# Kernel optimization log

Hardware: AMD Instinct MI355X
Metric: run time of the kernel (lower is better)

The kernel has to match this reference:

```python
import jax, jax.numpy as jnp
import numpy as np

NUM_HOPS = 2
GAMMA = 0.8


def setup_inputs() -> dict:
    key = jax.random.key(0)
    ks = jax.random.split(key, 17)
    B, L, V, E, M, Mt, R = 8, 128, 50257, 768, 400, 800, 40
    W = 0.02  # init scale for learned params
    return {
        'hidden_states': jax.random.normal(ks[0], (B, L, E), jnp.float32),
        'wte': jax.random.normal(ks[1], (V, E), jnp.float32) * W,
        'rel_emb': jax.random.normal(ks[2], (R, E), jnp.float32) * W,
        'W_s': jax.random.normal(ks[3], (NUM_HOPS, E, E), jnp.float32) * W,
        'W_n': jax.random.normal(ks[4], (NUM_HOPS, E, E), jnp.float32) * W,
        'W_r': jax.random.normal(ks[5], (NUM_HOPS, E, E), jnp.float32) * W,
        'W_triple': jax.random.normal(ks[6], (E, 3 * E), jnp.float32) * W,
        'gate_w': jax.random.normal(ks[7], (E,), jnp.float32) * W,
        'gate_b': jnp.zeros((), jnp.float32),
        'concept_ids': jax.random.randint(ks[8], (B, M), 0, V),
        'relation_ids': jax.random.randint(ks[9], (B, Mt), 0, R),
        'head_idx': jax.random.randint(ks[10], (B, Mt), 0, M),
        'tail_idx': jax.random.randint(ks[11], (B, Mt), 0, M),
        'triple_labels': jax.random.randint(ks[12], (B, Mt), 0, 2),
        'distances': jax.random.randint(ks[13], (B, M), 0, 3),
        'vocab_map': jax.random.randint(ks[14], (V,), 0, M),
        'map_mask': jax.random.randint(ks[15], (V,), 0, 2),
    }


def _triple_encoder(wte, rel_emb, W_s, W_n, W_r, concept_ids, relation_ids, head_idx, tail_idx):
    concept_repr = wte[concept_ids]      # B,M,E
    rel_repr = rel_emb[relation_ids]     # B,Mt,E

    def gcn(cr, rr, h, t):               # per-batch CompGCN, faithful to torch loop
        M = cr.shape[0]
        ch, rh = cr, rr
        for l in range(NUM_HOPS):
            upd = jnp.zeros_like(cr)
            upd = upd.at[t].add(cr[h] - rr)   # scatter_add(o) + scatter_add(-rel)
            upd = upd.at[h].add(cr[t] - rr)
            cnt = jnp.zeros((M,), cr.dtype).at[t].add(1.0).at[h].add(1.0)
            upd = cr @ W_s[l].T + (upd @ W_n[l].T) / jnp.clip(cnt, 1.0, None)[:, None]
            ch = jax.nn.relu(upd)
            rh = rr @ W_r[l].T
        return ch, rh

    node, relh = jax.vmap(gcn)(concept_repr, rel_repr, head_idx, tail_idx)
    E = node.shape[-1]
    hi = jnp.broadcast_to(head_idx[:, :, None], head_idx.shape + (E,))
    ti = jnp.broadcast_to(tail_idx[:, :, None], tail_idx.shape + (E,))
    hrep = jnp.take_along_axis(node, hi, axis=1)
    trep = jnp.take_along_axis(node, ti, axis=1)
    return jnp.concatenate([hrep, relh, trep], axis=-1)  # B,Mt,3E


def _multi_hop(triple_prob, distances, head, tail):
    B, L, Mt = triple_prob.shape
    M = distances.shape[1]
    dt = triple_prob.dtype
    init_mask = jnp.broadcast_to((distances == 0).astype(dt)[:, None, :], (B, L, M))
    decay = (0.8 ** distances.astype(dt))[:, None, :]
    head_b = jnp.broadcast_to(head[:, None, :], (B, L, Mt))

    def scatter_mean(vals, t):  # vals: L,Mt  t: Mt -> L,M
        s = jnp.zeros((L, M), vals.dtype).at[:, t].add(vals)
        c = jnp.zeros((M,), vals.dtype).at[t].add(1.0)
        return s / jnp.clip(c, 1.0, None)

    node_score = init_mask
    total = init_mask * (-100000.0)
    for _ in range(NUM_HOPS):
        ths = jnp.take_along_axis(node_score, head_b, axis=2)  # B,L,Mt
        upd = ths * GAMMA + triple_prob
        node_score = jax.vmap(scatter_mean)(upd, tail)          # B,L,M
        total = total + node_score * decay
    return total


def reference(hidden_states, wte, rel_emb, W_s, W_n, W_r, W_triple, gate_w, gate_b,
              concept_ids, relation_ids, head_idx, tail_idx, triple_labels,
              distances, vocab_map, map_mask):
    triple_repr = _triple_encoder(wte, rel_emb, W_s, W_n, W_r,
                                  concept_ids, relation_ids, head_idx, tail_idx)
    lm_probs = jax.nn.softmax(hidden_states @ wte.T, axis=-1)            # B,L,V
    tl = triple_repr @ W_triple.T                                        # B,Mt,E
    triple_prob = jax.nn.sigmoid(jnp.einsum('ble,bme->blm', hidden_states, tl))
    triple_prob = triple_prob * (triple_labels != -1)[:, None, :].astype(triple_prob.dtype)
    scores = _multi_hop(triple_prob, distances, head_idx, tail_idx)      # B,L,M
    concept_probs = jax.nn.softmax(scores, axis=-1)
    cpv = concept_probs[:, :, vocab_map]                                 # gather into vocab: B,L,V
    cpv = cpv * (map_mask != 0)[None, None, :].astype(cpv.dtype)
    gate = jax.nn.sigmoid(hidden_states @ gate_w + gate_b)[..., None]    # B,L,1
    probs = gate * cpv + (1.0 - gate) * lm_probs
    return probs
```

## Files before the change

kernel.cpp:

```cpp
#include <hip/hip_runtime.h>
#include <stdint.h>

#define HB 8
#define HL 128
#define HV 50257
#define HE 768
#define HM 400
#define HMT 800
#define HBL (HB*HL)
#define NTILES 393
#define ELD 50272
#define WTE_F4 ((long)HV*HE/4)

typedef __attribute__((ext_vector_type(4))) float f32x4;
typedef __attribute__((ext_vector_type(8))) short bf16x8;
typedef unsigned short u16;

struct u16x4 { u16 x, y, z, w; };

__device__ __forceinline__ u16 f2bf(float x){
  union { float f; uint32_t u; } v; v.f = x;
  uint32_t r = v.u + 0x7fffu + ((v.u >> 16) & 1u);
  return (u16)(r >> 16);
}
__device__ __forceinline__ float bf2f(u16 b){
  union { uint32_t u; float f; } v; v.u = ((uint32_t)b) << 16;
  return v.f;
}
__device__ __forceinline__ void glds(const u16* g, const u16* l){
  __builtin_amdgcn_global_load_lds(
      (const __attribute__((address_space(1))) void*)g,
      (__attribute__((address_space(3))) void*)l, 16, 0, 0);
}
__device__ __forceinline__ void cvt_slice(const float* __restrict__ src,
    u16* __restrict__ dst, long lo4, long n4, int relb, int nb){
  long i = lo4 + (long)relb*256 + threadIdx.x;
  const long end = lo4 + n4;
  const long stride = (long)nb*256;
  for (; i < end; i += stride) {
    float4 x = ((const float4*)src)[i];
    u16x4 y; y.x=f2bf(x.x); y.y=f2bf(x.y); y.z=f2bf(x.z); y.w=f2bf(x.w);
    ((u16x4*)dst)[i] = y;
  }
}

__global__ __launch_bounds__(256) void prep_k(const float* __restrict__ hs,
    const float* __restrict__ rel, const float* __restrict__ Wr1src,
    const float* __restrict__ Wt, const float* __restrict__ Ws1,
    const float* __restrict__ Wn1, const int* __restrict__ vmap,
    const int* __restrict__ mmask,
    u16* __restrict__ hid_b, u16* __restrict__ rel_b,
    u16* __restrict__ wr1, u16* __restrict__ wtT, u16* __restrict__ wcat,
    int* __restrict__ vmm){
  const int b = blockIdx.x, t = threadIdx.x;
  if (b < 768) {
    int i = b*256 + t;
    float4 x = ((const float4*)hs)[i];
    u16x4 y; y.x=f2bf(x.x); y.y=f2bf(x.y); y.z=f2bf(x.z); y.w=f2bf(x.w);
    ((u16x4*)hid_b)[i] = y;
  } else if (b < 798) {
    int i = (b-768)*256 + t;
    float4 x = ((const float4*)rel)[i];
    u16x4 y; y.x=f2bf(x.x); y.y=f2bf(x.y); y.z=f2bf(x.z); y.w=f2bf(x.w);
    ((u16x4*)rel_b)[i] = y;
  } else if (b < 1374) {
    int i = (b-798)*256 + t;
    float4 x = ((const float4*)Wr1src)[i];
    u16x4 y; y.x=f2bf(x.x); y.y=f2bf(x.y); y.z=f2bf(x.z); y.w=f2bf(x.w);
    ((u16x4*)wr1)[i] = y;
  } else if (b < 3102) {
    int g = (b-1374)*256 + t;
    int f = g / 192, r = g - f*192, e0 = r*4;
    u16x4 y;
    y.x = f2bf(Wt[(long)(e0+0)*2304 + f]);
    y.y = f2bf(Wt[(long)(e0+1)*2304 + f]);
    y.z = f2bf(Wt[(long)(e0+2)*2304 + f]);
    y.w = f2bf(Wt[(long)(e0+3)*2304 + f]);
    *(u16x4*)&wtT[(long)f*HE + e0] = y;
  } else if (b < 5406) {
    int i = (b-3102)*256 + t;
    int e = i / HE, k = i - e*HE;
    wcat[(long)e*(2*HE) + k]      = f2bf(Ws1[i]);
    wcat[(long)e*(2*HE) + HE + k] = f2bf(Wn1[i]);
  } else {
    int base = (b-5406)*1024 + t*4;
    #pragma unroll
    for (int i = 0; i < 4; ++i) {
      int c = base + i;
      if (c < HV) vmm[c] = mmask[c] ? vmap[c] : -1;
    }
  }
}

__global__ __launch_bounds__(256) void gcn_scatter_k(const float* __restrict__ wte,
    const float* __restrict__ rel, const int* __restrict__ cids,
    const int* __restrict__ rids, const int* __restrict__ head,
    const int* __restrict__ tail, u16* __restrict__ An,
    u16* __restrict__ wte_b){
  if (blockIdx.x >= 384) {
    cvt_slice(wte, wte_b, 0, 3145728L, blockIdx.x - 384, 3072);
    return;
  }
  const int ch = blockIdx.x % 48;
  const int b  = blockIdx.x / 48;
  const int e0 = ch * 16;
  __shared__ float cw[HM][17];
  __shared__ float upd[HM][17];
  __shared__ float relc[40][17];
  __shared__ float cnt[HM];
  const int tid = threadIdx.x;

  for (int idx = tid; idx < HM*16; idx += 256) {
    int m = idx >> 4, e = idx & 15;
    cw[m][e] = wte[(long)cids[b*HM+m]*HE + e0 + e];
    upd[m][e] = 0.f;
  }
  for (int idx = tid; idx < 40*16; idx += 256) {
    int r = idx >> 4, e = idx & 15;
    relc[r][e] = rel[r*HE + e0 + e];
  }
  for (int m = tid; m < HM; m += 256) cnt[m] = 0.f;
  __syncthreads();

  for (int j = tid; j < HMT; j += 256) {
    int h = head[b*HMT+j], t = tail[b*HMT+j], r = rids[b*HMT+j];
    atomicAdd(&cnt[t], 1.f);
    atomicAdd(&cnt[h], 1.f);
    #pragma unroll
    for (int e = 0; e < 16; ++e) {
      float rv = relc[r][e];
      atomicAdd(&upd[t][e], cw[h][e] - rv);
      atomicAdd(&upd[h][e], cw[t][e] - rv);
    }
  }
  __syncthreads();

  for (int idx = tid; idx < HM*16; idx += 256) {
    int m = idx >> 4, e = idx & 15;
    float ic = 1.f / fmaxf(cnt[m], 1.f);
    u16* dst = An + ((long)b*HM + m) * (2*HE);
    dst[e0 + e]      = f2bf(cw[m][e]);
    dst[HE + e0 + e] = f2bf(upd[m][e] * ic);
  }
}

template<int ACT, int OUTBF16, int BIG, int DBUF>
__device__ __forceinline__ void gemm_core(
    const u16* __restrict__ Ab, const u16* __restrict__ Bb,
    void* __restrict__ Cout, float* __restrict__ rowpart,
    int Mdim, int Ndim, int Kdim, int lda, int ldb, int ldc,
    int mtile, int ntile, u16* AsmB, u16* BsmB)
{
  const int m0 = mtile * 128;
  const int n0 = ntile * 128;
  const int tid = threadIdx.x;
  const int lane = tid & 63;
  const int wid = tid >> 6;
  const int wr = wid >> 1, wc = wid & 1;
  const int srw = lane >> 3;
  const int sl  = lane & 7;

  f32x4 acc[4][4] = {};

  auto stage = [&](int buf, int k0) {
    u16* As = AsmB + buf*8192;
    u16* Bs = BsmB + buf*8192;
    #pragma unroll
    for (int i = 0; i < 4; ++i) {
      const int c = i*4 + wid;
      const int row = c*8 + srw;
      const int koff = k0 + ((sl ^ srw) * 8);
      int ra = m0 + row; if (ra > Mdim-1) ra = Mdim-1;
      glds(Ab + (long)ra * lda + koff, &As[c*512]);
      int rn = n0 + row; if (rn > Ndim-1) rn = Ndim-1;
      glds(Bb + (long)rn * ldb + koff, &Bs[c*512]);
    }
  };
  auto compute = [&](int buf) {
    const u16* As = AsmB + buf*8192;
    const u16* Bs = BsmB + buf*8192;
    #pragma unroll
    for (int kk = 0; kk < 2; ++kk) {
      bf16x8 af[4], bfr[4];
      #pragma unroll
      for (int mi = 0; mi < 4; ++mi) {
        const int R = wr*64 + mi*16 + (lane & 15);
        af[mi] = *(const bf16x8*)&As[R*64 + (((kk*4 + (lane>>4)) ^ (R & 7)) * 8)];
      }
      #pragma unroll
      for (int ni = 0; ni < 4; ++ni) {
        const int R = wc*64 + ni*16 + (lane & 15);
        bfr[ni] = *(const bf16x8*)&Bs[R*64 + (((kk*4 + (lane>>4)) ^ (R & 7)) * 8)];
      }
      #pragma unroll
      for (int mi = 0; mi < 4; ++mi)
        #pragma unroll
        for (int ni = 0; ni < 4; ++ni)
          acc[mi][ni] = __builtin_amdgcn_mfma_f32_16x16x32_bf16(af[mi], bfr[ni], acc[mi][ni], 0, 0, 0);
    }
  };

  const int NT = Kdim >> 6;
  if (DBUF) {
    stage(0, 0);
    __syncthreads();
    int cur = 0;
    for (int t = 0; t < NT; ++t) {
      if (t + 1 < NT) stage(cur ^ 1, (t + 1) << 6);
      compute(cur);
      __syncthreads();
      cur ^= 1;
    }
  } else {
    for (int t = 0; t < NT; ++t) {
      stage(0, t << 6);
      __syncthreads();
      compute(0);
      __syncthreads();
    }
  }

  const int cr0 = m0 + wr*64 + ((lane >> 4) * 4);
  const int cc0 = n0 + wc*64 + (lane & 15);

  if (BIG) {
    float* rs = (float*)AsmB;
    #pragma unroll
    for (int mi = 0; mi < 4; ++mi) {
      #pragma unroll
      for (int r = 0; r < 4; ++r) {
        const int rowi = cr0 + mi*16 + r;
        float s = 0.f;
        #pragma unroll
        for (int ni = 0; ni < 4; ++ni) {
          const int col = cc0 + ni*16;
          if (col < Ndim) {
            float e = __expf(acc[mi][ni][r]);
            if (OUTBF16) ((u16*)Cout)[(long)rowi*ELD + col] = f2bf(e);
            else        ((float*)Cout)[(long)rowi*HV + col] = e;
            s += e;
          }
        }
        s += __shfl_xor(s, 8); s += __shfl_xor(s, 4);
        s += __shfl_xor(s, 2); s += __shfl_xor(s, 1);
        if ((lane & 15) == 0)
          rs[wc*128 + wr*64 + mi*16 + ((lane >> 4) << 2) + r] = s;
      }
    }
    __syncthreads();
    if (tid < 128)
      rowpart[(long)(m0 + tid) * NTILES + ntile] = rs[tid] + rs[128 + tid];
    return;
  }

  #pragma unroll
  for (int mi = 0; mi < 4; ++mi) {
    #pragma unroll
    for (int ni = 0; ni < 4; ++ni) {
      const int col = cc0 + ni*16;
      if (col < Ndim) {
        #pragma unroll
        for (int r = 0; r < 4; ++r) {
          const int rowi = cr0 + mi*16 + r;
          if (rowi < Mdim) {
            float v = acc[mi][ni][r];
            if (ACT == 1) v = fmaxf(v, 0.f);
            if (OUTBF16) ((u16*)Cout)[(long)rowi*ldc + col] = f2bf(v);
            else        ((float*)Cout)[(long)rowi*ldc + col] = v;
          }
        }
      }
    }
  }
}

template<int EXPBF>
__global__ __launch_bounds__(256) void gemm_big(
    const u16* __restrict__ hid_b, const u16* __restrict__ wte_b,
    void* __restrict__ expl, float* __restrict__ rowpart,
    int Mdim, int Ndim, int Kdim, int lda, int ldb, int ldc)
{
  __shared__ alignas(16) u16 Asm[8192];
  __shared__ alignas(16) u16 Bsm[8192];
  const int wg = (blockIdx.x & 7) * NTILES + (blockIdx.x >> 3);
  gemm_core<0,EXPBF,1,0>(hid_b, wte_b, expl, rowpart,
      Mdim, Ndim, Kdim, lda, ldb, ldc, wg & 7, wg >> 3, Asm, Bsm);
}

__global__ __launch_bounds__(256) void gemm_multi0(
    const u16* __restrict__ anode, const u16* __restrict__ wcat,
    u16* __restrict__ nodeb, const u16* __restrict__ rel_b,
    const u16* __restrict__ wr1, u16* __restrict__ relWr,
    const u16* __restrict__ hid_b, const u16* __restrict__ wtT,
    u16* __restrict__ hw, const float* __restrict__ wte,
    u16* __restrict__ wte_b)
{
  if (blockIdx.x >= 342) {
    cvt_slice(wte, wte_b, 3145728L, 4194304L, blockIdx.x - 342, 4096);
    return;
  }
  __shared__ alignas(16) u16 Asm[2*8192];
  __shared__ alignas(16) u16 Bsm[2*8192];
  const int q = blockIdx.x;
  if (q < 192) {
    const int z = q / 24, r = q - z*24;
    gemm_core<1,1,0,1>(anode + (long)z*HM*2*HE, wcat, nodeb + (long)z*HM*HE,
        nullptr, HM, HE, 2*HE, 2*HE, 2*HE, HE, r & 3, r >> 2, Asm, Bsm);
  } else if (q < 198) {
    gemm_core<0,1,0,1>(rel_b, wr1, relWr, nullptr,
        40, HE, HE, HE, HE, HE, 0, q - 192, Asm, Bsm);
  } else {
    const int u = q - 198;
    gemm_core<0,1,0,1>(hid_b, wtT, hw, nullptr,
        HBL, 3*HE, HE, HE, HE, 3*HE, u & 7, u >> 3, Asm, Bsm);
  }
}

__global__ __launch_bounds__(256) void gemm_multi1(
    const u16* __restrict__ hw, const u16* __restrict__ nodeb,
    const u16* __restrict__ relWr, float* __restrict__ scores,
    const float* __restrict__ wte, u16* __restrict__ wte_b)
{
  if (blockIdx.x >= 72) {
    cvt_slice(wte, wte_b, 7340032L, 1048576L, blockIdx.x - 72, 1024);
    return;
  }
  __shared__ alignas(16) u16 Asm[2*8192];
  __shared__ alignas(16) u16 Bsm[2*8192];
  const int q = blockIdx.x;
  if (q < 32) {
    const int z = q >> 2;
    gemm_core<0,0,0,1>(hw + (long)z*HL*(3*HE), nodeb + (long)z*HM*HE,
        scores + (long)z*HL*840, nullptr,
        HL, HM, HE, 3*HE, HE, 840, 0, q & 3, Asm, Bsm);
  } else if (q < 64) {
    const int z = (q - 32) >> 2;
    gemm_core<0,0,0,1>(hw + (long)z*HL*(3*HE) + 2*HE, nodeb + (long)z*HM*HE,
        scores + (long)z*HL*840 + HM, nullptr,
        HL, HM, HE, 3*HE, HE, 840, 0, (q - 32) & 3, Asm, Bsm);
  } else {
    gemm_core<0,0,0,1>(hw + HE, relWr, scores + 2*HM, nullptr,
        HBL, 40, HE, 3*HE, HE, 840, q - 64, 0, Asm, Bsm);
  }
}

__global__ __launch_bounds__(256) void multihop_k(const float* __restrict__ scores,
    const float* __restrict__ hs, const float* __restrict__ gw,
    const float* __restrict__ gb,
    const int* __restrict__ head, const int* __restrict__ tail,
    const int* __restrict__ rids, const int* __restrict__ labels,
    const int* __restrict__ dist, float* __restrict__ gatev,
    float* __restrict__ cprob, const float* __restrict__ wte,
    u16* __restrict__ wte_b){
  if (blockIdx.x >= HBL) {
    cvt_slice(wte, wte_b, 8388608L, WTE_F4 - 8388608L, blockIdx.x - HBL, 1280);
    return;
  }
  const int bl = blockIdx.x;
  const int b = bl >> 7;
  const int tid = threadIdx.x;
  const int lane = tid & 63, wid = tid >> 6;
  __shared__ float srow[840];
  __shared__ float tp[HMT];
  __shared__ float ns[HM], sacc[HM], tot[HM], invc[HM], dec[HM];
  __shared__ float red[16];
  __shared__ float gred[4];
  const int* hb = head + b*HMT;
  const int* tb = tail + b*HMT;
  const int* rb = rids + b*HMT;
  const int* lb = labels + b*HMT;
  const float* sr = scores + (long)bl * 840;

  float gs = 0.f;
  for (int e = tid; e < HE; e += 256) gs += hs[(long)bl*HE + e] * gw[e];
  for (int o = 32; o; o >>= 1) gs += __shfl_down(gs, o);
  if (lane == 0) gred[wid] = gs;

  for (int i = tid; i < 840; i += 256) srow[i] = sr[i];
  for (int m = tid; m < HM; m += 256) {
    int d = dist[b*HM + m];
    float im = (d == 0) ? 1.f : 0.f;
    ns[m] = im; tot[m] = im * -100000.f;
    dec[m] = (d == 0) ? 1.f : ((d == 1) ? 0.8f : 0.64f);
    sacc[m] = 0.f; invc[m] = 0.f;
  }
  __syncthreads();
  if (tid == 0)
    gatev[bl] = 1.f / (1.f + __expf(-(gred[0]+gred[1]+gred[2]+gred[3] + gb[0])));
  for (int j = tid; j < HMT; j += 256) {
    atomicAdd(&invc[tb[j]], 1.f);
    float x = srow[hb[j]] + srow[HM + tb[j]] + srow[2*HM + rb[j]];
    tp[j] = (lb[j] == -1) ? 0.f : 1.f / (1.f + __expf(-x));
  }
  __syncthreads();
  for (int m = tid; m < HM; m += 256) invc[m] = 1.f / fmaxf(invc[m], 1.f);
  __syncthreads();

  for (int hop = 0; hop < 2; ++hop) {
    for (int j = tid; j < HMT; j += 256) {
      float u = ns[hb[j]] * 0.8f + tp[j];
      atomicAdd(&sacc[tb[j]], u);
    }
    __syncthreads();
    for (int m = tid; m < HM; m += 256) {
      float v = sacc[m] * invc[m];
      ns[m] = v; tot[m] += v * dec[m]; sacc[m] = 0.f;
    }
    __syncthreads();
  }

  float lmx = -3.4e38f;
  for (int m = tid; m < HM; m += 256) lmx = fmaxf(lmx, tot[m]);
  for (int o = 32; o; o >>= 1) lmx = fmaxf(lmx, __shfl_down(lmx, o));
  if (lane == 0) red[wid] = lmx;
  __syncthreads();
  float gmx = fmaxf(fmaxf(red[0], red[1]), fmaxf(red[2], red[3]));
  float ls = 0.f;
  for (int m = tid; m < HM; m += 256) ls += __expf(tot[m] - gmx);
  for (int o = 32; o; o >>= 1) ls += __shfl_down(ls, o);
  if (lane == 0) red[8 + wid] = ls;
  __syncthreads();
  float inv = 1.f / (red[8] + red[9] + red[10] + red[11]);
  float* outrow = cprob + (long)bl * HM;
  for (int m = tid; m < HM; m += 256) outrow[m] = __expf(tot[m] - gmx) * inv;
}

template<int EXPBF>
__global__ __launch_bounds__(256) void finalize_k(const void* __restrict__ expl,
    const float* __restrict__ rowpart, const float* __restrict__ gatev,
    const float* __restrict__ cprob, const int* __restrict__ vmm,
    float* __restrict__ out){
  const int r = blockIdx.x / 13;
  const int ch = blockIdx.x - r*13;
  const int tid = threadIdx.x;
  __shared__ float red[4];
  __shared__ float cpl[HM];
  float s = 0.f;
  for (int t = tid; t < NTILES; t += 256) s += rowpart[r*NTILES + t];
  for (int o = 32; o; o >>= 1) s += __shfl_down(s, o);
  if ((tid & 63) == 0) red[tid >> 6] = s;
  const float g = gatev[r];
  for (int m = tid; m < HM; m += 256) cpl[m] = g * cprob[r*HM + m];
  __syncthreads();
  const float scale = (1.f - g) / (red[0] + red[1] + red[2] + red[3]);
  const u16* erb = (const u16*)expl + (long)r * ELD;
  const float* erf = (const float*)expl + (long)r * HV;
  float* orow = out + (long)r * HV;
  #pragma unroll
  for (int it = 0; it < 2; ++it) {
    const int c = ch*4096 + it*2048 + tid*8;
    if (c + 8 <= HV) {
      float e[8];
      if (EXPBF) {
        bf16x8 v = *(const bf16x8*)&erb[c];
        #pragma unroll
        for (int i = 0; i < 8; ++i) e[i] = bf2f((u16)v[i]);
      } else {
        float4 a = *(const float4*)&erf[c];
        float4 b2 = *(const float4*)&erf[c+4];
        e[0]=a.x; e[1]=a.y; e[2]=a.z; e[3]=a.w;
        e[4]=b2.x; e[5]=b2.y; e[6]=b2.z; e[7]=b2.w;
      }
      int4 v0 = *(const int4*)&vmm[c];
      int4 v1 = *(const int4*)&vmm[c+4];
      const int ix[8] = {v0.x, v0.y, v0.z, v0.w, v1.x, v1.y, v1.z, v1.w};
      float o8[8];
      #pragma unroll
      for (int i = 0; i < 8; ++i)
        o8[i] = (ix[i] >= 0 ? cpl[ix[i]] : 0.f) + scale * e[i];
      *(float4*)&orow[c]   = make_float4(o8[0], o8[1], o8[2], o8[3]);
      *(float4*)&orow[c+4] = make_float4(o8[4], o8[5], o8[6], o8[7]);
    } else if (c < HV) {
      for (int i = 0; i < 8 && c + i < HV; ++i) {
        float e = EXPBF ? bf2f(((const u16*)expl)[(long)r*ELD + c + i]) : erf[c+i];
        int ix = vmm[c+i];
        orow[c+i] = (ix >= 0 ? cpl[ix] : 0.f) + scale * e;
      }
    }
  }
}

extern "C" void kernel_launch(void* const* d_in, const int* in_sizes, int n_in,
                              void* d_out, int out_size, void* d_ws, size_t ws_size,
                              hipStream_t stream)
{
  const float* hs   = (const float*)d_in[0];
  const float* wte  = (const float*)d_in[1];
  const float* rel  = (const float*)d_in[2];
  const float* Ws   = (const float*)d_in[3];
  const float* Wn   = (const float*)d_in[4];
  const float* Wr   = (const float*)d_in[5];
  const float* Wt   = (const float*)d_in[6];
  const float* gw   = (const float*)d_in[7];
  const float* gb   = (const float*)d_in[8];
  const int* cids   = (const int*)d_in[9];
  const int* rids   = (const int*)d_in[10];
  const int* head   = (const int*)d_in[11];
  const int* tail   = (const int*)d_in[12];
  const int* labels = (const int*)d_in[13];
  const int* dist   = (const int*)d_in[14];
  const int* vmap   = (const int*)d_in[15];
  const int* mmask  = (const int*)d_in[16];
  float* out = (float*)d_out;

  char* ws = (char*)d_ws;
  size_t o = 0;
  auto alloc = [&](size_t bytes) -> char* {
    char* p = ws + o; o = (o + bytes + 255) & ~(size_t)255; return p;
  };
  u16* wte_b     = (u16*)alloc((size_t)HV*HE*2);
  u16* hid_b     = (u16*)alloc((size_t)HBL*HE*2);
  float* cprob   = (float*)alloc((size_t)HBL*HM*4);
  float* rowpart = (float*)alloc((size_t)HBL*NTILES*4);
  float* gatev   = (float*)alloc(HBL*4);
  int* vmm       = (int*)alloc((size_t)HV*4);
  float* scores  = (float*)alloc((size_t)HBL*840*4);

  const bool bigws = ws_size >= (size_t)196*1024*1024;
  u16* expl = (u16*)(ws + o);
  u16* wcat  = (u16*)alloc((size_t)HE*2*HE*2);
  u16* wr1   = (u16*)alloc((size_t)HE*HE*2);
  u16* wtT   = (u16*)alloc((size_t)3*HE*HE*2);
  u16* rel_b = (u16*)alloc((size_t)40*HE*2);
  u16* anode = (u16*)alloc((size_t)HB*HM*2*HE*2);
  u16* nodeb = (u16*)alloc((size_t)HB*HM*HE*2);
  u16* relWr = (u16*)alloc((size_t)40*HE*2);
  u16* hw    = (u16*)alloc((size_t)HBL*3*HE*2);
  (void)in_sizes; (void)n_in; (void)out_size;

  prep_k<<<5456, 256, 0, stream>>>(hs, rel, Wr + (size_t)HE*HE, Wt,
      Ws + (size_t)HE*HE, Wn + (size_t)HE*HE, vmap, mmask,
      hid_b, rel_b, wr1, wtT, wcat, vmm);

  gcn_scatter_k<<<384 + 3072, 256, 0, stream>>>(wte, rel, cids, rids, head,
      tail, anode, wte_b);

  gemm_multi0<<<342 + 4096, 256, 0, stream>>>(anode, wcat, nodeb, rel_b, wr1,
      relWr, hid_b, wtT, hw, wte, wte_b);
  gemm_multi1<<<72 + 1024, 256, 0, stream>>>(hw, nodeb, relWr, scores,
      wte, wte_b);

  multihop_k<<<HBL + 1280, 256, 0, stream>>>(scores, hs, gw, gb, head, tail,
      rids, labels, dist, gatev, cprob, wte, wte_b);

  if (bigws) {
    gemm_big<1><<<3144, 256, 0, stream>>>(hid_b, wte_b, expl, rowpart,
        HBL, HV, HE, HE, HE, ELD);
    finalize_k<1><<<HBL*13, 256, 0, stream>>>(expl, rowpart, gatev, cprob,
        vmm, out);
  } else {
    gemm_big<0><<<3144, 256, 0, stream>>>(hid_b, wte_b, out, rowpart,
        HBL, HV, HE, HE, HE, HV);
    finalize_k<0><<<HBL*13, 256, 0, stream>>>(out, rowpart, gatev, cprob,
        vmm, out);
  }
}
```

Measured before the change: 398.1 us.

## Specialize big vocab GEMM with K=32 double-buffered tiles, merge prep and scatter kernels

The large logits GEMM gets its own kernel. It uses double-buffered K=32 stages through direct global-to-LDS loads and swaps the MFMA operands so each lane holds four consecutive columns, which allows vectorized 4-wide exp stores and a cheaper row-sum reduction. The prep kernel and the GCN scatter kernel are merged into a single launch to cut one kernel boundary. The wte conversion slices are rebalanced across the preceding launches. The changes trade LDS footprint and sync frequency (more K iterations) for overlap and wider stores.

```diff
diff --git a/kernel.cpp b/kernel.cpp
--- a/kernel.cpp
+++ b/kernel.cpp
@@ -44,61 +44,61 @@
   }
 }
 
-__global__ __launch_bounds__(256) void prep_k(const float* __restrict__ hs,
-    const float* __restrict__ rel, const float* __restrict__ Wr1src,
+__global__ __launch_bounds__(256) void gcn_prep_k(const float* __restrict__ wte,
+    const float* __restrict__ rel, const int* __restrict__ cids,
+    const int* __restrict__ rids, const int* __restrict__ head,
+    const int* __restrict__ tail, u16* __restrict__ An,
+    const float* __restrict__ hs, const float* __restrict__ Wr1src,
     const float* __restrict__ Wt, const float* __restrict__ Ws1,
     const float* __restrict__ Wn1, const int* __restrict__ vmap,
     const int* __restrict__ mmask,
     u16* __restrict__ hid_b, u16* __restrict__ rel_b,
     u16* __restrict__ wr1, u16* __restrict__ wtT, u16* __restrict__ wcat,
-    int* __restrict__ vmm){
-  const int b = blockIdx.x, t = threadIdx.x;
-  if (b < 768) {
-    int i = b*256 + t;
-    float4 x = ((const float4*)hs)[i];
-    u16x4 y; y.x=f2bf(x.x); y.y=f2bf(x.y); y.z=f2bf(x.z); y.w=f2bf(x.w);
-    ((u16x4*)hid_b)[i] = y;
-  } else if (b < 798) {
-    int i = (b-768)*256 + t;
-    float4 x = ((const float4*)rel)[i];
-    u16x4 y; y.x=f2bf(x.x); y.y=f2bf(x.y); y.z=f2bf(x.z); y.w=f2bf(x.w);
-    ((u16x4*)rel_b)[i] = y;
-  } else if (b < 1374) {
-    int i = (b-798)*256 + t;
-    float4 x = ((const float4*)Wr1src)[i];
-    u16x4 y; y.x=f2bf(x.x); y.y=f2bf(x.y); y.z=f2bf(x.z); y.w=f2bf(x.w);
-    ((u16x4*)wr1)[i] = y;
-  } else if (b < 3102) {
-    int g = (b-1374)*256 + t;
-    int f = g / 192, r = g - f*192, e0 = r*4;
-    u16x4 y;
-    y.x = f2bf(Wt[(long)(e0+0)*2304 + f]);
-    y.y = f2bf(Wt[(long)(e0+1)*2304 + f]);
-    y.z = f2bf(Wt[(long)(e0+2)*2304 + f]);
-    y.w = f2bf(Wt[(long)(e0+3)*2304 + f]);
-    *(u16x4*)&wtT[(long)f*HE + e0] = y;
-  } else if (b < 5406) {
-    int i = (b-3102)*256 + t;
-    int e = i / HE, k = i - e*HE;
-    wcat[(long)e*(2*HE) + k]      = f2bf(Ws1[i]);
-    wcat[(long)e*(2*HE) + HE + k] = f2bf(Wn1[i]);
-  } else {
-    int base = (b-5406)*1024 + t*4;
-    #pragma unroll
-    for (int i = 0; i < 4; ++i) {
-      int c = base + i;
-      if (c < HV) vmm[c] = mmask[c] ? vmap[c] : -1;
-    }
-  }
-}
-
-__global__ __launch_bounds__(256) void gcn_scatter_k(const float* __restrict__ wte,
-    const float* __restrict__ rel, const int* __restrict__ cids,
-    const int* __restrict__ rids, const int* __restrict__ head,
-    const int* __restrict__ tail, u16* __restrict__ An,
-    u16* __restrict__ wte_b){
+    int* __restrict__ vmm, u16* __restrict__ wte_b){
+  const int t = threadIdx.x;
+  if (blockIdx.x >= 5840) {
+    cvt_slice(wte, wte_b, 0, 2621440L, blockIdx.x - 5840, 2048);
+    return;
+  }
   if (blockIdx.x >= 384) {
-    cvt_slice(wte, wte_b, 0, 3145728L, blockIdx.x - 384, 3072);
+    const int b = blockIdx.x - 384;
+    if (b < 768) {
+      int i = b*256 + t;
+      float4 x = ((const float4*)hs)[i];
+      u16x4 y; y.x=f2bf(x.x); y.y=f2bf(x.y); y.z=f2bf(x.z); y.w=f2bf(x.w);
+      ((u16x4*)hid_b)[i] = y;
+    } else if (b < 798) {
+      int i = (b-768)*256 + t;
+      float4 x = ((const float4*)rel)[i];
+      u16x4 y; y.x=f2bf(x.x); y.y=f2bf(x.y); y.z=f2bf(x.z); y.w=f2bf(x.w);
+      ((u16x4*)rel_b)[i] = y;
+    } else if (b < 1374) {
+      int i = (b-798)*256 + t;
+      float4 x = ((const float4*)Wr1src)[i];
+      u16x4 y; y.x=f2bf(x.x); y.y=f2bf(x.y); y.z=f2bf(x.z); y.w=f2bf(x.w);
+      ((u16x4*)wr1)[i] = y;
+    } else if (b < 3102) {
+      int g = (b-1374)*256 + t;
+      int f = g / 192, r = g - f*192, e0 = r*4;
+      u16x4 y;
+      y.x = f2bf(Wt[(long)(e0+0)*2304 + f]);
+      y.y = f2bf(Wt[(long)(e0+1)*2304 + f]);
+      y.z = f2bf(Wt[(long)(e0+2)*2304 + f]);
+      y.w = f2bf(Wt[(long)(e0+3)*2304 + f]);
+      *(u16x4*)&wtT[(long)f*HE + e0] = y;
+    } else if (b < 5406) {
+      int i = (b-3102)*256 + t;
+      int e = i / HE, k = i - e*HE;
+      wcat[(long)e*(2*HE) + k]      = f2bf(Ws1[i]);
+      wcat[(long)e*(2*HE) + HE + k] = f2bf(Wn1[i]);
+    } else {
+      int base = (b-5406)*1024 + t*4;
+      #pragma unroll
+      for (int i = 0; i < 4; ++i) {
+        int c = base + i;
+        if (c < HV) vmm[c] = mmask[c] ? vmap[c] : -1;
+      }
+    }
     return;
   }
   const int ch = blockIdx.x % 48;
@@ -108,7 +108,7 @@
   __shared__ float upd[HM][17];
   __shared__ float relc[40][17];
   __shared__ float cnt[HM];
-  const int tid = threadIdx.x;
+  const int tid = t;
 
   for (int idx = tid; idx < HM*16; idx += 256) {
     int m = idx >> 4, e = idx & 15;
@@ -123,14 +123,14 @@
   __syncthreads();
 
   for (int j = tid; j < HMT; j += 256) {
-    int h = head[b*HMT+j], t = tail[b*HMT+j], r = rids[b*HMT+j];
-    atomicAdd(&cnt[t], 1.f);
+    int h = head[b*HMT+j], tt = tail[b*HMT+j], r = rids[b*HMT+j];
+    atomicAdd(&cnt[tt], 1.f);
     atomicAdd(&cnt[h], 1.f);
     #pragma unroll
     for (int e = 0; e < 16; ++e) {
       float rv = relc[r][e];
-      atomicAdd(&upd[t][e], cw[h][e] - rv);
-      atomicAdd(&upd[h][e], cw[t][e] - rv);
+      atomicAdd(&upd[tt][e], cw[h][e] - rv);
+      atomicAdd(&upd[h][e], cw[tt][e] - rv);
     }
   }
   __syncthreads();
@@ -144,10 +144,10 @@
   }
 }
 
-template<int ACT, int OUTBF16, int BIG, int DBUF>
+template<int ACT, int OUTBF16, int DBUF>
 __device__ __forceinline__ void gemm_core(
     const u16* __restrict__ Ab, const u16* __restrict__ Bb,
-    void* __restrict__ Cout, float* __restrict__ rowpart,
+    void* __restrict__ Cout,
     int Mdim, int Ndim, int Kdim, int lda, int ldb, int ldc,
     int mtile, int ntile, u16* AsmB, u16* BsmB)
 {
@@ -222,37 +222,6 @@
 
   const int cr0 = m0 + wr*64 + ((lane >> 4) * 4);
   const int cc0 = n0 + wc*64 + (lane & 15);
-
-  if (BIG) {
-    float* rs = (float*)AsmB;
-    #pragma unroll
-    for (int mi = 0; mi < 4; ++mi) {
-      #pragma unroll
-      for (int r = 0; r < 4; ++r) {
-        const int rowi = cr0 + mi*16 + r;
-        float s = 0.f;
-        #pragma unroll
-        for (int ni = 0; ni < 4; ++ni) {
-          const int col = cc0 + ni*16;
-          if (col < Ndim) {
-            float e = __expf(acc[mi][ni][r]);
-            if (OUTBF16) ((u16*)Cout)[(long)rowi*ELD + col] = f2bf(e);
-            else        ((float*)Cout)[(long)rowi*HV + col] = e;
-            s += e;
-          }
-        }
-        s += __shfl_xor(s, 8); s += __shfl_xor(s, 4);
-        s += __shfl_xor(s, 2); s += __shfl_xor(s, 1);
-        if ((lane & 15) == 0)
-          rs[wc*128 + wr*64 + mi*16 + ((lane >> 4) << 2) + r] = s;
-      }
-    }
-    __syncthreads();
-    if (tid < 128)
-      rowpart[(long)(m0 + tid) * NTILES + ntile] = rs[tid] + rs[128 + tid];
-    return;
-  }
-
   #pragma unroll
   for (int mi = 0; mi < 4; ++mi) {
     #pragma unroll
@@ -276,15 +245,106 @@
 
 template<int EXPBF>
 __global__ __launch_bounds__(256) void gemm_big(
-    const u16* __restrict__ hid_b, const u16* __restrict__ wte_b,
-    void* __restrict__ expl, float* __restrict__ rowpart,
+    const u16* __restrict__ A, const u16* __restrict__ Bm,
+    void* __restrict__ Cout, float* __restrict__ rowpart,
     int Mdim, int Ndim, int Kdim, int lda, int ldb, int ldc)
 {
-  __shared__ alignas(16) u16 Asm[8192];
-  __shared__ alignas(16) u16 Bsm[8192];
+  __shared__ alignas(16) u16 Asm[2*4096];
+  __shared__ alignas(16) u16 Bsm[2*4096];
   const int wg = (blockIdx.x & 7) * NTILES + (blockIdx.x >> 3);
-  gemm_core<0,EXPBF,1,0>(hid_b, wte_b, expl, rowpart,
-      Mdim, Ndim, Kdim, lda, ldb, ldc, wg & 7, wg >> 3, Asm, Bsm);
+  const int m0 = (wg & 7) * 128;
+  const int n0 = (wg >> 3) * 128;
+  const int ntile = wg >> 3;
+  const int tid = threadIdx.x;
+  const int lane = tid & 63;
+  const int wid = tid >> 6;
+  const int wr = wid >> 1, wc = wid & 1;
+  const int srow = lane >> 2;
+  const int sl = lane & 3;
+
+  f32x4 acc[4][4] = {};
+
+  auto stage = [&](int buf, int k0) {
+    u16* As = Asm + buf*4096;
+    u16* Bs = Bsm + buf*4096;
+    #pragma unroll
+    for (int i = 0; i < 2; ++i) {
+      const int c = i*4 + wid;
+      const int row = c*16 + srow;
+      const int koff = k0 + sl*8;
+      int ra = m0 + row; if (ra > Mdim-1) ra = Mdim-1;
+      glds(A + (long)ra*lda + koff, &As[c*512]);
+      int rn = n0 + row; if (rn > Ndim-1) rn = Ndim-1;
+      glds(Bm + (long)rn*ldb + koff, &Bs[c*512]);
+    }
+  };
+  auto compute = [&](int buf) {
+    const u16* As = Asm + buf*4096;
+    const u16* Bs = Bsm + buf*4096;
+    bf16x8 af[4], bfr[4];
+    #pragma unroll
+    for (int mi = 0; mi < 4; ++mi)
+      af[mi] = *(const bf16x8*)&As[(wr*64 + mi*16 + (lane&15))*32 + (lane>>4)*8];
+    #pragma unroll
+    for (int ni = 0; ni < 4; ++ni)
+      bfr[ni] = *(const bf16x8*)&Bs[(wc*64 + ni*16 + (lane&15))*32 + (lane>>4)*8];
+    #pragma unroll
+    for (int ni = 0; ni < 4; ++ni)
+      #pragma unroll
+      for (int mi = 0; mi < 4; ++mi)
+        acc[ni][mi] = __builtin_amdgcn_mfma_f32_16x16x32_bf16(bfr[ni], af[mi], acc[ni][mi], 0, 0, 0);
+  };
+
+  const int NT = Kdim >> 5;
+  stage(0, 0);
+  __syncthreads();
+  int cur = 0;
+  for (int t = 0; t < NT; ++t) {
+    if (t + 1 < NT) stage(cur ^ 1, (t + 1) << 5);
+    compute(cur);
+    __syncthreads();
+    cur ^= 1;
+  }
+
+  const int f = lane & 15;
+  float* rs = (float*)Asm;
+  #pragma unroll
+  for (int mi = 0; mi < 4; ++mi) {
+    const int rowi = m0 + wr*64 + mi*16 + f;
+    float s = 0.f;
+    #pragma unroll
+    for (int ni = 0; ni < 4; ++ni) {
+      const int cb = n0 + wc*64 + ni*16 + (lane >> 4)*4;
+      f32x4 a = acc[ni][mi];
+      float e0 = __expf(a[0]), e1 = __expf(a[1]);
+      float e2 = __expf(a[2]), e3 = __expf(a[3]);
+      if (cb + 3 < Ndim) {
+        s += e0 + e1 + e2 + e3;
+        if (EXPBF) {
+          ushort4 y; y.x=f2bf(e0); y.y=f2bf(e1); y.z=f2bf(e2); y.w=f2bf(e3);
+          *(ushort4*)&((u16*)Cout)[(long)rowi*ldc + cb] = y;
+        } else {
+          float* dst = &((float*)Cout)[(long)rowi*ldc + cb];
+          dst[0]=e0; dst[1]=e1; dst[2]=e2; dst[3]=e3;
+        }
+      } else {
+        float ev[4] = {e0, e1, e2, e3};
+        for (int i = 0; i < 4; ++i) {
+          if (cb + i < Ndim) {
+            s += ev[i];
+            if (EXPBF) ((u16*)Cout)[(long)rowi*ldc + cb + i] = f2bf(ev[i]);
+            else      ((float*)Cout)[(long)rowi*ldc + cb + i] = ev[i];
+          }
+        }
+      }
+    }
+    s += __shfl_xor(s, 16);
+    s += __shfl_xor(s, 32);
+    if ((lane >> 4) == 0) rs[wc*128 + wr*64 + mi*16 + f] = s;
+  }
+  __syncthreads();
+  if (tid < 128)
+    rowpart[(long)(m0 + tid) * NTILES + ntile] = rs[tid] + rs[128 + tid];
 }
 
 __global__ __launch_bounds__(256) void gemm_multi0(
@@ -296,7 +356,7 @@
     u16* __restrict__ wte_b)
 {
   if (blockIdx.x >= 342) {
-    cvt_slice(wte, wte_b, 3145728L, 4194304L, blockIdx.x - 342, 4096);
+    cvt_slice(wte, wte_b, 2621440L, 4194304L, blockIdx.x - 342, 4096);
     return;
   }
   __shared__ alignas(16) u16 Asm[2*8192];
@@ -304,14 +364,14 @@
   const int q = blockIdx.x;
   if (q < 192) {
     const int z = q / 24, r = q - z*24;
-    gemm_core<1,1,0,1>(anode + (long)z*HM*2*HE, wcat, nodeb + (long)z*HM*HE,
-        nullptr, HM, HE, 2*HE, 2*HE, 2*HE, HE, r & 3, r >> 2, Asm, Bsm);
+    gemm_core<1,1,1>(anode + (long)z*HM*2*HE, wcat, nodeb + (long)z*HM*HE,
+        HM, HE, 2*HE, 2*HE, 2*HE, HE, r & 3, r >> 2, Asm, Bsm);
   } else if (q < 198) {
-    gemm_core<0,1,0,1>(rel_b, wr1, relWr, nullptr,
+    gemm_core<0,1,1>(rel_b, wr1, relWr,
         40, HE, HE, HE, HE, HE, 0, q - 192, Asm, Bsm);
   } else {
     const int u = q - 198;
-    gemm_core<0,1,0,1>(hid_b, wtT, hw, nullptr,
+    gemm_core<0,1,1>(hid_b, wtT, hw,
         HBL, 3*HE, HE, HE, HE, 3*HE, u & 7, u >> 3, Asm, Bsm);
   }
 }
@@ -322,7 +382,7 @@
     const float* __restrict__ wte, u16* __restrict__ wte_b)
 {
   if (blockIdx.x >= 72) {
-    cvt_slice(wte, wte_b, 7340032L, 1048576L, blockIdx.x - 72, 1024);
+    cvt_slice(wte, wte_b, 6815744L, 1572864L, blockIdx.x - 72, 1536);
     return;
   }
   __shared__ alignas(16) u16 Asm[2*8192];
@@ -330,16 +390,16 @@
   const int q = blockIdx.x;
   if (q < 32) {
     const int z = q >> 2;
-    gemm_core<0,0,0,1>(hw + (long)z*HL*(3*HE), nodeb + (long)z*HM*HE,
-        scores + (long)z*HL*840, nullptr,
+    gemm_core<0,0,1>(hw + (long)z*HL*(3*HE), nodeb + (long)z*HM*HE,
+        scores + (long)z*HL*840,
         HL, HM, HE, 3*HE, HE, 840, 0, q & 3, Asm, Bsm);
   } else if (q < 64) {
     const int z = (q - 32) >> 2;
-    gemm_core<0,0,0,1>(hw + (long)z*HL*(3*HE) + 2*HE, nodeb + (long)z*HM*HE,
-        scores + (long)z*HL*840 + HM, nullptr,
+    gemm_core<0,0,1>(hw + (long)z*HL*(3*HE) + 2*HE, nodeb + (long)z*HM*HE,
+        scores + (long)z*HL*840 + HM,
         HL, HM, HE, 3*HE, HE, 840, 0, (q - 32) & 3, Asm, Bsm);
   } else {
-    gemm_core<0,0,0,1>(hw + HE, relWr, scores + 2*HM, nullptr,
+    gemm_core<0,0,1>(hw + HE, relWr, scores + 2*HM,
         HBL, 40, HE, 3*HE, HE, 840, q - 64, 0, Asm, Bsm);
   }
 }
@@ -528,16 +588,14 @@
   u16* hw    = (u16*)alloc((size_t)HBL*3*HE*2);
   (void)in_sizes; (void)n_in; (void)out_size;
 
-  prep_k<<<5456, 256, 0, stream>>>(hs, rel, Wr + (size_t)HE*HE, Wt,
-      Ws + (size_t)HE*HE, Wn + (size_t)HE*HE, vmap, mmask,
-      hid_b, rel_b, wr1, wtT, wcat, vmm);
-
-  gcn_scatter_k<<<384 + 3072, 256, 0, stream>>>(wte, rel, cids, rids, head,
-      tail, anode, wte_b);
+  gcn_prep_k<<<5840 + 2048, 256, 0, stream>>>(wte, rel, cids, rids, head,
+      tail, anode, hs, Wr + (size_t)HE*HE, Wt, Ws + (size_t)HE*HE,
+      Wn + (size_t)HE*HE, vmap, mmask,
+      hid_b, rel_b, wr1, wtT, wcat, vmm, wte_b);
 
   gemm_multi0<<<342 + 4096, 256, 0, stream>>>(anode, wcat, nodeb, rel_b, wr1,
       relWr, hid_b, wtT, hw, wte, wte_b);
-  gemm_multi1<<<72 + 1024, 256, 0, stream>>>(hw, nodeb, relWr, scores,
+  gemm_multi1<<<72 + 1536, 256, 0, stream>>>(hw, nodeb, relWr, scores,
       wte, wte_b);
 
   multihop_k<<<HBL + 1280, 256, 0, stream>>>(scores, hs, gw, gb, head, tail,
```

After: 384.9 us. 1.03x faster.
